# Kernel optimization log

Hardware: AMD Instinct MI355X
Metric: run time of the kernel (lower is better)

Reference implementation:

```python
import jax, jax.numpy as jnp
import numpy as np

B, S, HID = 2, 2048, 2048
NH, NKV, HD = 16, 4, 128
G = NH // NKV  # kv group size
EPS = 1e-6


def setup_inputs() -> dict:
    key = jax.random.key(0)
    ks = jax.random.split(key, 7)
    w = 0.02
    return {
        "hidden_states": jax.random.normal(ks[0], (B, S, HID), dtype=jnp.float32),
        "position_ids": jnp.broadcast_to(jnp.arange(S, dtype=jnp.int64), (B, S)),
        "Wq": jax.random.normal(ks[1], (2 * NH * HD, HID), dtype=jnp.float32) * w,
        "Wk": jax.random.normal(ks[2], (NKV * HD, HID), dtype=jnp.float32) * w,
        "Wv": jax.random.normal(ks[3], (NKV * HD, HID), dtype=jnp.float32) * w,
        "Wo": jax.random.normal(ks[4], (HID, NH * HD), dtype=jnp.float32) * w,
        "norm_w": jnp.zeros((HID,), dtype=jnp.float32),
    }


def reference(hidden_states, position_ids, Wq, Wk, Wv, Wo, norm_w):
    # RMSNorm (weight parameterized as 1 + w, per source)
    ms = jnp.mean(hidden_states * hidden_states, axis=-1, keepdims=True)
    x = hidden_states * jax.lax.rsqrt(ms + EPS) * (1.0 + norm_w)

    qg = x @ Wq.T                                   # (B,S,2*NH*HD)
    q, gate = jnp.split(qg, 2, axis=-1)
    q = q.reshape(B, S, NH, HD).transpose(0, 2, 1, 3)       # (B,NH,S,HD)
    gate = gate.reshape(B, S, NH, HD).transpose(0, 2, 1, 3)
    k = (x @ Wk.T).reshape(B, S, NKV, HD).transpose(0, 2, 1, 3)  # (B,NKV,S,HD)
    v = (x @ Wv.T).reshape(B, S, NKV, HD).transpose(0, 2, 1, 3)

    scale = 1.0 / np.sqrt(HD).astype(np.float32)
    qg4 = q.reshape(B, NKV, G, S, HD)
    attn = jnp.einsum("bkgqd,bkld->bkgql", qg4, k) * scale   # (B,NKV,G,S,S)
    p = jax.nn.softmax(attn, axis=-1)
    o = jnp.einsum("bkgql,bkld->bkgqd", p, v).reshape(B, NH, S, HD)

    o = o * jax.nn.sigmoid(gate)                    # output gate
    o = o.transpose(0, 2, 1, 3).reshape(B, S, NH * HD)
    return o @ Wo.T
```

## Files before the change

kernel.cpp:

```cpp
#include <hip/hip_runtime.h>
#include <math.h>

#define BB    2
#define SS    2048
#define HIDD  2048
#define NHH   16
#define NKVV  4
#define HDD   128
#define MROWS 4096
#define QG_N  4096
#define KV_N  512
#define O_N   2048
#define KDIM  2048
#define EPS_  1e-6f
#define SCALE_ 0.08838834764831845f

typedef __attribute__((ext_vector_type(8))) __bf16 bf16x8;
typedef __attribute__((ext_vector_type(8))) unsigned short u16x8;
typedef __attribute__((ext_vector_type(4))) float f32x4;

__device__ __forceinline__ unsigned short f2bf(float f) {
  return __builtin_bit_cast(unsigned short, (__bf16)f);
}

__global__ __launch_bounds__(256) void f2bf_k(const float* __restrict__ in,
                                              unsigned short* __restrict__ out, int n4) {
  int i = blockIdx.x * 256 + threadIdx.x;
  if (i < n4) {
    float4 v = ((const float4*)in)[i];
    ushort4 u;
    u.x = f2bf(v.x); u.y = f2bf(v.y); u.z = f2bf(v.z); u.w = f2bf(v.w);
    ((ushort4*)out)[i] = u;
  }
}

__global__ __launch_bounds__(256) void rmsnorm_k(const float* __restrict__ h,
                                                 const float* __restrict__ w,
                                                 unsigned short* __restrict__ x) {
  int row = blockIdx.x;
  int t = threadIdx.x;
  const float4* hr = (const float4*)(h + (size_t)row * HIDD);
  const float4* w4 = (const float4*)w;

  float4 v0 = hr[t], v1 = hr[t + 256];
  float ss = v0.x*v0.x + v0.y*v0.y + v0.z*v0.z + v0.w*v0.w
           + v1.x*v1.x + v1.y*v1.y + v1.z*v1.z + v1.w*v1.w;
#pragma unroll
  for (int off = 32; off > 0; off >>= 1) ss += __shfl_down(ss, off, 64);

  __shared__ float part[4];
  __shared__ float rs_sh;
  if ((t & 63) == 0) part[t >> 6] = ss;
  __syncthreads();
  if (t == 0) rs_sh = rsqrtf((part[0]+part[1]+part[2]+part[3]) * (1.0f/HIDD) + EPS_);
  __syncthreads();
  float rs = rs_sh;

  float4 w0 = w4[t], w1 = w4[t + 256];
  ushort4 o0, o1;
  o0.x = f2bf(v0.x * rs * (1.f + w0.x));
  o0.y = f2bf(v0.y * rs * (1.f + w0.y));
  o0.z = f2bf(v0.z * rs * (1.f + w0.z));
  o0.w = f2bf(v0.w * rs * (1.f + w0.w));
  o1.x = f2bf(v1.x * rs * (1.f + w1.x));
  o1.y = f2bf(v1.y * rs * (1.f + w1.y));
  o1.z = f2bf(v1.z * rs * (1.f + w1.z));
  o1.w = f2bf(v1.w * rs * (1.f + w1.w));
  ushort4* xr = (ushort4*)(x + (size_t)row * HIDD);
  xr[t] = o0;
  xr[t + 256] = o1;
}

template <int OBF>
__device__ __forceinline__ void gemm_core(const unsigned short* __restrict__ Ab,
                                          const unsigned short* __restrict__ Bb,
                                          void* __restrict__ Cv,
                                          int Ndim, int bm, int bn,
                                          unsigned short* Als, unsigned short* Bls) {
  char* ldsA = (char*)Als;
  char* ldsB = (char*)Bls;

  int t   = threadIdx.x;
  int r15 = t & 15;
  int g   = (t & 63) >> 4;
  int w   = t >> 6;
  int wr  = w >> 1, wc = w & 1;

  f32x4 acc[4][4] = {};

  for (int k0 = 0; k0 < KDIM; k0 += 64) {
    __syncthreads();
#pragma unroll
    for (int it = 0; it < 4; ++it) {
      int f      = it * 256 + t;
      int row    = f >> 3;
      int schunk = (f & 7) ^ (row & 7);
      unsigned ldsbase = (unsigned)((it * 256 + (w << 6)) << 4);
      __builtin_amdgcn_global_load_lds(
          (const unsigned int*)(Ab + ((size_t)(bm + row) << 11) + k0 + schunk * 8),
          (unsigned int*)(ldsA + ldsbase), 16, 0, 0);
      __builtin_amdgcn_global_load_lds(
          (const unsigned int*)(Bb + ((size_t)(bn + row) << 11) + k0 + schunk * 8),
          (unsigned int*)(ldsB + ldsbase), 16, 0, 0);
    }
    __syncthreads();

#pragma unroll
    for (int tt = 0; tt < 2; ++tt) {
      bf16x8 af[4], bfv[4];
#pragma unroll
      for (int mi = 0; mi < 4; ++mi) {
        int row = wr * 64 + mi * 16 + r15;
        af[mi] = *(const bf16x8*)(ldsA + row * 128 + (((4 * tt + g) ^ (row & 7)) << 4));
      }
#pragma unroll
      for (int ni = 0; ni < 4; ++ni) {
        int row = wc * 64 + ni * 16 + r15;
        bfv[ni] = *(const bf16x8*)(ldsB + row * 128 + (((4 * tt + g) ^ (row & 7)) << 4));
      }
#pragma unroll
      for (int mi = 0; mi < 4; ++mi)
#pragma unroll
        for (int ni = 0; ni < 4; ++ni)
          acc[mi][ni] = __builtin_amdgcn_mfma_f32_16x16x32_bf16(af[mi], bfv[ni], acc[mi][ni], 0, 0, 0);
    }
  }

#pragma unroll
  for (int mi = 0; mi < 4; ++mi)
#pragma unroll
    for (int ni = 0; ni < 4; ++ni) {
      int col = bn + wc * 64 + ni * 16 + r15;
#pragma unroll
      for (int r = 0; r < 4; ++r) {
        int rowg = bm + wr * 64 + mi * 16 + g * 4 + r;
        if (OBF)
          ((unsigned short*)Cv)[(size_t)rowg * Ndim + col] = f2bf(acc[mi][ni][r]);
        else
          ((float*)Cv)[(size_t)rowg * Ndim + col] = acc[mi][ni][r];
      }
    }
}

template <int OBF>
__global__ __launch_bounds__(256) void gemm_bf16(const unsigned short* __restrict__ Ab,
                                                 const unsigned short* __restrict__ Bb,
                                                 void* __restrict__ Cv,
                                                 int Ndim) {
  __shared__ unsigned short Als[128 * 64];
  __shared__ unsigned short Bls[128 * 64];
  gemm_core<OBF>(Ab, Bb, Cv, Ndim, blockIdx.y * 128, blockIdx.x * 128, Als, Bls);
}

__global__ __launch_bounds__(256) void gemm_kv(const unsigned short* __restrict__ Ab,
                                               const unsigned short* __restrict__ Wk,
                                               const unsigned short* __restrict__ Wv,
                                               unsigned short* __restrict__ Ck,
                                               unsigned short* __restrict__ Cva) {
  __shared__ unsigned short Als[128 * 64];
  __shared__ unsigned short Bls[128 * 64];
  int bx = blockIdx.x;
  const unsigned short* Bb = (bx < 4) ? Wk : Wv;
  unsigned short* Cv = (bx < 4) ? Ck : Cva;
  gemm_core<1>(Ab, Bb, (void*)Cv, KV_N, blockIdx.y * 128, (bx & 3) * 128, Als, Bls);
}

__global__ __launch_bounds__(256, 2) void attn_mfma(const float* __restrict__ qg,
                                                    const unsigned short* __restrict__ kb,
                                                    const unsigned short* __restrict__ vb,
                                                    unsigned short* __restrict__ obuf) {
  __shared__ unsigned short Ks[2][64 * 128];
  __shared__ unsigned short Vt[2][64 * 128];
  __shared__ unsigned short Ps[4][32 * 64];
  char* ldsK0 = (char*)Ks;
  char* ldsV0 = (char*)Vt;

  int t = threadIdx.x;
  int l = t & 63, w = t >> 6;
  int c15 = l & 15, g = l >> 4;
  char* ldsP = (char*)(Ps[w]);
  int qt = blockIdx.x, h = blockIdx.y, b = blockIdx.z;
  int kh = h >> 2;
  size_t rowQ0 = (size_t)b * SS + (size_t)qt * 128;
  size_t rowKbase = (size_t)b * SS;

  bf16x8 qf[2][4];
#pragma unroll
  for (int qi = 0; qi < 2; ++qi)
#pragma unroll
    for (int ks = 0; ks < 4; ++ks) {
      int d0 = g * 8 + ks * 32;
      const float* qp = qg + (rowQ0 + w * 32 + qi * 16 + c15) * QG_N + h * HDD + d0;
      float4 a = *(const float4*)qp;
      float4 c = *(const float4*)(qp + 4);
      bf16x8 q8;
      q8[0] = (__bf16)(a.x * SCALE_); q8[1] = (__bf16)(a.y * SCALE_);
      q8[2] = (__bf16)(a.z * SCALE_); q8[3] = (__bf16)(a.w * SCALE_);
      q8[4] = (__bf16)(c.x * SCALE_); q8[5] = (__bf16)(c.y * SCALE_);
      q8[6] = (__bf16)(c.z * SCALE_); q8[7] = (__bf16)(c.w * SCALE_);
      qf[qi][ks] = q8;
    }

  f32x4 accO[2][8] = {};
  float mrun[2] = {-INFINITY, -INFINITY};
  float lrun[2] = {0.f, 0.f};
  u16x8 vreg[4];

#define ISSUE_K(bufi, kt_)                                                     \
  {                                                                            \
    size_t rowK0 = rowKbase + (size_t)(kt_) * 64;                              \
    _Pragma("unroll")                                                          \
    for (int it = 0; it < 4; ++it) {                                           \
      int f = it * 256 + t;                                                    \
      int kv = f >> 4;                                                         \
      int schunk = (f & 15) ^ (kv & 7);                                        \
      unsigned ldsbase = (unsigned)((it * 256 + (w << 6)) << 4);               \
      __builtin_amdgcn_global_load_lds(                                        \
          (const unsigned int*)(kb + (rowK0 + kv) * KV_N + kh * HDD + schunk * 8), \
          (unsigned int*)(ldsK0 + (bufi) * 16384 + ldsbase), 16, 0, 0);        \
    }                                                                          \
  }
#define ISSUE_V(kt_)                                                           \
  {                                                                            \
    size_t rowK0 = rowKbase + (size_t)(kt_) * 64;                              \
    _Pragma("unroll")                                                          \
    for (int it = 0; it < 4; ++it) {                                           \
      int f = it * 256 + t;                                                    \
      int kv = f & 63;                                                         \
      int d8 = (f >> 6) * 8;                                                   \
      vreg[it] = *(const u16x8*)(vb + (rowK0 + kv) * KV_N + kh * HDD + d8);    \
    }                                                                          \
  }
#define WRITE_V(bufi)                                                          \
  {                                                                            \
    _Pragma("unroll")                                                          \
    for (int it = 0; it < 4; ++it) {                                           \
      int f = it * 256 + t;                                                    \
      int kv = f & 63;                                                         \
      int d8 = (f >> 6) * 8;                                                   \
      _Pragma("unroll")                                                        \
      for (int i = 0; i < 8; ++i) {                                            \
        int d = d8 + i;                                                        \
        *(unsigned short*)(ldsV0 + (bufi) * 16384 + d * 128 +                  \
                           (((kv >> 3) ^ (d & 7)) << 4) + (kv & 7) * 2) = vreg[it][i]; \
      }                                                                        \
    }                                                                          \
  }

  ISSUE_K(0, 0);
  ISSUE_V(0);
  asm volatile("s_waitcnt vmcnt(0)" ::: "memory");
  WRITE_V(0);
  __syncthreads();

  const int NT = SS / 64;
  for (int kt = 0; kt < NT; ++kt) {
    int cur = kt & 1, nxt = cur ^ 1;
    char* ldsK = ldsK0 + cur * 16384;
    char* ldsV = ldsV0 + cur * 16384;

    if (kt + 1 < NT) {
      ISSUE_K(nxt, kt + 1);
      ISSUE_V(kt + 1);
    }

    f32x4 accS[2][4] = {};
#pragma unroll
    for (int nf = 0; nf < 4; ++nf) {
      int kvr = nf * 16 + c15;
#pragma unroll
      for (int ks = 0; ks < 4; ++ks) {
        bf16x8 kf = *(const bf16x8*)(ldsK + kvr * 256 + ((((g + 4 * ks) ^ (kvr & 7)) << 4)));
#pragma unroll
        for (int qi = 0; qi < 2; ++qi)
          accS[qi][nf] = __builtin_amdgcn_mfma_f32_16x16x32_bf16(kf, qf[qi][ks], accS[qi][nf], 0, 0, 0);
      }
    }

    float mt[2];
#pragma unroll
    for (int qi = 0; qi < 2; ++qi) {
      float m0 = fmaxf(fmaxf(accS[qi][0][0], accS[qi][0][1]), fmaxf(accS[qi][0][2], accS[qi][0][3]));
#pragma unroll
      for (int nf = 1; nf < 4; ++nf)
        m0 = fmaxf(m0, fmaxf(fmaxf(accS[qi][nf][0], accS[qi][nf][1]), fmaxf(accS[qi][nf][2], accS[qi][nf][3])));
      m0 = fmaxf(m0, __shfl_xor(m0, 16, 64));
      m0 = fmaxf(m0, __shfl_xor(m0, 32, 64));
      mt[qi] = m0;
    }

    bool safe = (mt[0] <= mrun[0] + 8.f) && (mt[1] <= mrun[1] + 8.f);
    if (!__all(safe)) {
#pragma unroll
      for (int qi = 0; qi < 2; ++qi) {
        float mnew = fmaxf(mrun[qi], mt[qi]);
        float al = __expf(mrun[qi] - mnew);
        mrun[qi] = mnew;
        lrun[qi] *= al;
        float alr[4];
#pragma unroll
        for (int r = 0; r < 4; ++r) alr[r] = __shfl(al, g * 4 + r, 16);
#pragma unroll
        for (int df = 0; df < 8; ++df)
#pragma unroll
          for (int r = 0; r < 4; ++r) accO[qi][df][r] *= alr[r];
      }
    }

#pragma unroll
    for (int qi = 0; qi < 2; ++qi) {
      float ps = 0.f;
#pragma unroll
      for (int nf = 0; nf < 4; ++nf) {
        float p0 = __expf(accS[qi][nf][0] - mrun[qi]);
        float p1 = __expf(accS[qi][nf][1] - mrun[qi]);
        float p2 = __expf(accS[qi][nf][2] - mrun[qi]);
        float p3 = __expf(accS[qi][nf][3] - mrun[qi]);
        ps += (p0 + p1) + (p2 + p3);
        ushort4 pk;
        pk.x = f2bf(p0); pk.y = f2bf(p1); pk.z = f2bf(p2); pk.w = f2bf(p3);
        int q = qi * 16 + c15;
        *(ushort4*)(ldsP + q * 128 + ((((nf << 2) + g) ^ (q & 15)) << 3)) = pk;
      }
      ps += __shfl_xor(ps, 16, 64);
      ps += __shfl_xor(ps, 32, 64);
      lrun[qi] += ps;
    }
    asm volatile("s_waitcnt lgkmcnt(0)" ::: "memory");

#pragma unroll
    for (int ks2 = 0; ks2 < 2; ++ks2) {
      bf16x8 pf[2];
#pragma unroll
      for (int qi = 0; qi < 2; ++qi) {
        int q = qi * 16 + c15;
        int ch0 = ((ks2 << 3) + (g << 1)) ^ (q & 15);
        int ch1 = ((ks2 << 3) + (g << 1) + 1) ^ (q & 15);
        ushort4 lo = *(const ushort4*)(ldsP + q * 128 + (ch0 << 3));
        ushort4 hi = *(const ushort4*)(ldsP + q * 128 + (ch1 << 3));
        u16x8 p8 = {lo.x, lo.y, lo.z, lo.w, hi.x, hi.y, hi.z, hi.w};
        pf[qi] = __builtin_bit_cast(bf16x8, p8);
      }
#pragma unroll
      for (int df = 0; df < 8; ++df) {
        int d = df * 16 + c15;
        bf16x8 vf = *(const bf16x8*)(ldsV + d * 128 + ((((g + 4 * ks2) ^ (d & 7)) << 4)));
#pragma unroll
        for (int qi = 0; qi < 2; ++qi)
          accO[qi][df] = __builtin_amdgcn_mfma_f32_16x16x32_bf16(pf[qi], vf, accO[qi][df], 0, 0, 0);
      }
    }

    if (kt + 1 < NT) {
      asm volatile("s_waitcnt vmcnt(0)" ::: "memory");
      WRITE_V(nxt);
    }
    __syncthreads();
  }

#pragma unroll
  for (int qi = 0; qi < 2; ++qi) {
    float invL = 1.f / lrun[qi];
    float ivr[4];
#pragma unroll
    for (int r = 0; r < 4; ++r) ivr[r] = __shfl(invL, g * 4 + r, 16);
#pragma unroll
    for (int r = 0; r < 4; ++r) {
      size_t row = rowQ0 + w * 32 + qi * 16 + g * 4 + r;
#pragma unroll
      for (int df = 0; df < 8; ++df) {
        int d = df * 16 + c15;
        float gt = qg[row * QG_N + O_N + h * HDD + d];
        float sg = 1.f / (1.f + __expf(-gt));
        obuf[row * (size_t)O_N + h * HDD + d] = f2bf(accO[qi][df][r] * ivr[r] * sg);
      }
    }
  }
#undef ISSUE_K
#undef ISSUE_V
#undef WRITE_V
}

extern "C" void kernel_launch(void* const* d_in, const int* in_sizes, int n_in,
                              void* d_out, int out_size, void* d_ws, size_t ws_size,
                              hipStream_t stream) {
  const float* hs = (const float*)d_in[0];
  const float* Wq = (const float*)d_in[2];
  const float* Wk = (const float*)d_in[3];
  const float* Wv = (const float*)d_in[4];
  const float* Wo = (const float*)d_in[5];
  const float* nw = (const float*)d_in[6];
  float* out = (float*)d_out;

  float* qgb = (float*)d_ws;
  unsigned short* kb16 = (unsigned short*)(qgb + (size_t)MROWS * QG_N);
  unsigned short* vb16 = kb16 + (size_t)MROWS * KV_N;
  unsigned short* xb   = vb16 + (size_t)MROWS * KV_N;
  unsigned short* ob   = xb   + (size_t)MROWS * HIDD;
  unsigned short* wqb  = ob   + (size_t)MROWS * O_N;
  unsigned short* wkb  = wqb  + (size_t)QG_N * KDIM;
  unsigned short* wvb  = wkb  + (size_t)KV_N * KDIM;
  unsigned short* wob  = wvb  + (size_t)KV_N * KDIM;

  f2bf_k<<<(QG_N*KDIM/4 + 255)/256, 256, 0, stream>>>(Wq, wqb, QG_N*KDIM/4);
  f2bf_k<<<(KV_N*KDIM/4 + 255)/256, 256, 0, stream>>>(Wk, wkb, KV_N*KDIM/4);
  f2bf_k<<<(KV_N*KDIM/4 + 255)/256, 256, 0, stream>>>(Wv, wvb, KV_N*KDIM/4);
  f2bf_k<<<(O_N*KDIM/4  + 255)/256, 256, 0, stream>>>(Wo, wob, O_N*KDIM/4);
  rmsnorm_k<<<MROWS, 256, 0, stream>>>(hs, nw, xb);

  gemm_bf16<0><<<dim3(QG_N/128, MROWS/128), 256, 0, stream>>>(xb, wqb, qgb, QG_N);
  gemm_kv<<<dim3(8, MROWS/128), 256, 0, stream>>>(xb, wkb, wvb, kb16, vb16);
  attn_mfma<<<dim3(SS/128, NHH, BB), 256, 0, stream>>>(qgb, kb16, vb16, ob);
  gemm_bf16<0><<<dim3(O_N/128, MROWS/128), 256, 0, stream>>>(ob, wob, out, O_N);
}
```

Before: 296.3 us.

## Emit scaled bf16 Q from QG GEMM, swizzle attention blocks, raise MFMA priority

The Q/gate GEMM epilogue now writes Q as pre-scaled bf16 into its own buffer and the gate as fp32 into a separate buffer. This halves the Q traffic and removes the per-element conversion in the attention kernel. The attention launch becomes a 1D grid with a swizzle so that blocks scheduled together are spread across heads and batches, likely to improve K/V cache locality across dies. s_setprio raises wave priority around MFMA loops in both the GEMM and the attention kernels. Rounding Q to bf16 after scaling slightly changes numerics.

```diff
diff --git a/kernel.cpp b/kernel.cpp
--- a/kernel.cpp
+++ b/kernel.cpp
@@ -75,6 +75,7 @@
 __device__ __forceinline__ void gemm_core(const unsigned short* __restrict__ Ab,
                                           const unsigned short* __restrict__ Bb,
                                           void* __restrict__ Cv,
+                                          void* __restrict__ Cv2,
                                           int Ndim, int bm, int bn,
                                           unsigned short* Als, unsigned short* Bls) {
   char* ldsA = (char*)Als;
@@ -118,11 +119,13 @@
         int row = wc * 64 + ni * 16 + r15;
         bfv[ni] = *(const bf16x8*)(ldsB + row * 128 + (((4 * tt + g) ^ (row & 7)) << 4));
       }
+      __builtin_amdgcn_s_setprio(1);
 #pragma unroll
       for (int mi = 0; mi < 4; ++mi)
 #pragma unroll
         for (int ni = 0; ni < 4; ++ni)
           acc[mi][ni] = __builtin_amdgcn_mfma_f32_16x16x32_bf16(af[mi], bfv[ni], acc[mi][ni], 0, 0, 0);
+      __builtin_amdgcn_s_setprio(0);
     }
   }
 
@@ -134,9 +137,14 @@
 #pragma unroll
       for (int r = 0; r < 4; ++r) {
         int rowg = bm + wr * 64 + mi * 16 + g * 4 + r;
-        if (OBF)
+        if (OBF == 1)
           ((unsigned short*)Cv)[(size_t)rowg * Ndim + col] = f2bf(acc[mi][ni][r]);
-        else
+        else if (OBF == 2) {
+          if (col < O_N)
+            ((unsigned short*)Cv)[(size_t)rowg * O_N + col] = f2bf(acc[mi][ni][r] * SCALE_);
+          else
+            ((float*)Cv2)[(size_t)rowg * O_N + (col - O_N)] = acc[mi][ni][r];
+        } else
           ((float*)Cv)[(size_t)rowg * Ndim + col] = acc[mi][ni][r];
       }
     }
@@ -149,7 +157,16 @@
                                                  int Ndim) {
   __shared__ unsigned short Als[128 * 64];
   __shared__ unsigned short Bls[128 * 64];
-  gemm_core<OBF>(Ab, Bb, Cv, Ndim, blockIdx.y * 128, blockIdx.x * 128, Als, Bls);
+  gemm_core<OBF>(Ab, Bb, Cv, nullptr, Ndim, blockIdx.y * 128, blockIdx.x * 128, Als, Bls);
+}
+
+__global__ __launch_bounds__(256) void gemm_qg(const unsigned short* __restrict__ Ab,
+                                               const unsigned short* __restrict__ Bb,
+                                               unsigned short* __restrict__ Cq,
+                                               float* __restrict__ Cg) {
+  __shared__ unsigned short Als[128 * 64];
+  __shared__ unsigned short Bls[128 * 64];
+  gemm_core<2>(Ab, Bb, (void*)Cq, (void*)Cg, QG_N, blockIdx.y * 128, blockIdx.x * 128, Als, Bls);
 }
 
 __global__ __launch_bounds__(256) void gemm_kv(const unsigned short* __restrict__ Ab,
@@ -162,10 +179,11 @@
   int bx = blockIdx.x;
   const unsigned short* Bb = (bx < 4) ? Wk : Wv;
   unsigned short* Cv = (bx < 4) ? Ck : Cva;
-  gemm_core<1>(Ab, Bb, (void*)Cv, KV_N, blockIdx.y * 128, (bx & 3) * 128, Als, Bls);
-}
-
-__global__ __launch_bounds__(256, 2) void attn_mfma(const float* __restrict__ qg,
+  gemm_core<1>(Ab, Bb, (void*)Cv, nullptr, KV_N, blockIdx.y * 128, (bx & 3) * 128, Als, Bls);
+}
+
+__global__ __launch_bounds__(256, 2) void attn_mfma(const unsigned short* __restrict__ qb,
+                                                    const float* __restrict__ gateb,
                                                     const unsigned short* __restrict__ kb,
                                                     const unsigned short* __restrict__ vb,
                                                     unsigned short* __restrict__ obuf) {
@@ -179,7 +197,9 @@
   int l = t & 63, w = t >> 6;
   int c15 = l & 15, g = l >> 4;
   char* ldsP = (char*)(Ps[w]);
-  int qt = blockIdx.x, h = blockIdx.y, b = blockIdx.z;
+  int bid = blockIdx.x;
+  int swz = (bid & 7) * 64 + (bid >> 3);
+  int qt = swz & 15, h = (swz >> 4) & 15, b = swz >> 8;
   int kh = h >> 2;
   size_t rowQ0 = (size_t)b * SS + (size_t)qt * 128;
   size_t rowKbase = (size_t)b * SS;
@@ -188,18 +208,9 @@
 #pragma unroll
   for (int qi = 0; qi < 2; ++qi)
 #pragma unroll
-    for (int ks = 0; ks < 4; ++ks) {
-      int d0 = g * 8 + ks * 32;
-      const float* qp = qg + (rowQ0 + w * 32 + qi * 16 + c15) * QG_N + h * HDD + d0;
-      float4 a = *(const float4*)qp;
-      float4 c = *(const float4*)(qp + 4);
-      bf16x8 q8;
-      q8[0] = (__bf16)(a.x * SCALE_); q8[1] = (__bf16)(a.y * SCALE_);
-      q8[2] = (__bf16)(a.z * SCALE_); q8[3] = (__bf16)(a.w * SCALE_);
-      q8[4] = (__bf16)(c.x * SCALE_); q8[5] = (__bf16)(c.y * SCALE_);
-      q8[6] = (__bf16)(c.z * SCALE_); q8[7] = (__bf16)(c.w * SCALE_);
-      qf[qi][ks] = q8;
-    }
+    for (int ks = 0; ks < 4; ++ks)
+      qf[qi][ks] = *(const bf16x8*)(qb + (rowQ0 + w * 32 + qi * 16 + c15) * O_N
+                                       + h * HDD + g * 8 + ks * 32);
 
   f32x4 accO[2][8] = {};
   float mrun[2] = {-INFINITY, -INFINITY};
@@ -265,6 +276,7 @@
     }
 
     f32x4 accS[2][4] = {};
+    __builtin_amdgcn_s_setprio(1);
 #pragma unroll
     for (int nf = 0; nf < 4; ++nf) {
       int kvr = nf * 16 + c15;
@@ -276,6 +288,7 @@
           accS[qi][nf] = __builtin_amdgcn_mfma_f32_16x16x32_bf16(kf, qf[qi][ks], accS[qi][nf], 0, 0, 0);
       }
     }
+    __builtin_amdgcn_s_setprio(0);
 
     float mt[2];
 #pragma unroll
@@ -328,6 +341,7 @@
     }
     asm volatile("s_waitcnt lgkmcnt(0)" ::: "memory");
 
+    __builtin_amdgcn_s_setprio(1);
 #pragma unroll
     for (int ks2 = 0; ks2 < 2; ++ks2) {
       bf16x8 pf[2];
@@ -350,6 +364,7 @@
           accO[qi][df] = __builtin_amdgcn_mfma_f32_16x16x32_bf16(pf[qi], vf, accO[qi][df], 0, 0, 0);
       }
     }
+    __builtin_amdgcn_s_setprio(0);
 
     if (kt + 1 < NT) {
       asm volatile("s_waitcnt vmcnt(0)" ::: "memory");
@@ -370,7 +385,7 @@
 #pragma unroll
       for (int df = 0; df < 8; ++df) {
         int d = df * 16 + c15;
-        float gt = qg[row * QG_N + O_N + h * HDD + d];
+        float gt = gateb[row * (size_t)O_N + h * HDD + d];
         float sg = 1.f / (1.f + __expf(-gt));
         obuf[row * (size_t)O_N + h * HDD + d] = f2bf(accO[qi][df][r] * ivr[r] * sg);
       }
@@ -392,8 +407,9 @@
   const float* nw = (const float*)d_in[6];
   float* out = (float*)d_out;
 
-  float* qgb = (float*)d_ws;
-  unsigned short* kb16 = (unsigned short*)(qgb + (size_t)MROWS * QG_N);
+  float* gateb = (float*)d_ws;
+  unsigned short* qb16 = (unsigned short*)(gateb + (size_t)MROWS * O_N);
+  unsigned short* kb16 = qb16 + (size_t)MROWS * O_N;
   unsigned short* vb16 = kb16 + (size_t)MROWS * KV_N;
   unsigned short* xb   = vb16 + (size_t)MROWS * KV_N;
   unsigned short* ob   = xb   + (size_t)MROWS * HIDD;
@@ -408,8 +424,8 @@
   f2bf_k<<<(O_N*KDIM/4  + 255)/256, 256, 0, stream>>>(Wo, wob, O_N*KDIM/4);
   rmsnorm_k<<<MROWS, 256, 0, stream>>>(hs, nw, xb);
 
-  gemm_bf16<0><<<dim3(QG_N/128, MROWS/128), 256, 0, stream>>>(xb, wqb, qgb, QG_N);
+  gemm_qg<<<dim3(QG_N/128, MROWS/128), 256, 0, stream>>>(xb, wqb, qb16, gateb);
   gemm_kv<<<dim3(8, MROWS/128), 256, 0, stream>>>(xb, wkb, wvb, kb16, vb16);
-  attn_mfma<<<dim3(SS/128, NHH, BB), 256, 0, stream>>>(qgb, kb16, vb16, ob);
+  attn_mfma<<<dim3(512), 256, 0, stream>>>(qb16, gateb, kb16, vb16, ob);
   gemm_bf16<0><<<dim3(O_N/128, MROWS/128), 256, 0, stream>>>(ob, wob, out, O_N);
 }
```

After: 292.3 us. About the same (-1.3%).
